# Performance work log

Hardware: AMD Instinct MI355X
Metric: run time of the kernel (lower is better)

Reference implementation:

```python
import jax, jax.numpy as jnp
import numpy as np

N = 100000      # num_nodes (num_users + num_items)
E = 1600000     # directed edges after symmetrization
DIN = 256
HID = 64
DOUT = 64


def setup_inputs() -> dict:
    key = jax.random.key(0)
    k = jax.random.split(key, 4)
    x = jax.random.normal(k[0], (N, DIN), dtype=jnp.float32)
    edge_index = jax.random.randint(k[1], (2, E), 0, N)
    edge_weight = jnp.ones((E,), dtype=jnp.float32)
    W1 = jax.random.normal(k[2], (DIN, HID), dtype=jnp.float32) * (1.0 / np.sqrt(DIN))
    b1 = jnp.zeros((HID,), dtype=jnp.float32)
    W2 = jax.random.normal(k[3], (HID, DOUT), dtype=jnp.float32) * (1.0 / np.sqrt(HID))
    b2 = jnp.zeros((DOUT,), dtype=jnp.float32)
    return {"x": x, "edge_index": edge_index, "edge_weight": edge_weight,
            "W1": W1, "b1": b1, "W2": W2, "b2": b2}


def _gcn_layer(x, W, b, src, dst, ew):
    # PyG GCNConv: h = x @ W; symmetric degree normalization; scatter-add at dst; + bias
    h = x @ W                                             # [N, D_out]
    deg = jax.ops.segment_sum(ew, dst, num_segments=N)    # in-degree w.r.t. edge weights
    dinv = jnp.where(deg > 0, jax.lax.rsqrt(deg), 0.0)    # deg^{-1/2}, inf -> 0
    norm = dinv[src] * ew * dinv[dst]                     # [E_tot]
    msg = h[src] * norm[:, None]                          # gather + scale
    out = jax.ops.segment_sum(msg, dst, num_segments=N)   # scatter-add
    return out + b


def reference(x, edge_index, edge_weight, W1, b1, W2, b2):
    # add self-loops with weight 1 (GCNConv default add_self_loops=True)
    loop = jnp.arange(N, dtype=edge_index.dtype)
    src = jnp.concatenate([edge_index[0], loop])
    dst = jnp.concatenate([edge_index[1], loop])
    ew = jnp.concatenate([edge_weight, jnp.ones((N,), edge_weight.dtype)])
    h = jax.nn.relu(_gcn_layer(x, W1, b1, src, dst, ew))
    return _gcn_layer(h, W2, b2, src, dst, ew)
```

## Files before the change

kernel.cpp:

```cpp
#include <hip/hip_runtime.h>
#include <math.h>


#define GCN_DIN 256
#define GCN_HID 64
#define SCAN_B 1024
#define PCHUNK 4096
#define NBMAX 256

__global__ void count_kernel(const int* __restrict__ dst, int* __restrict__ counts, int E) {
    int e = blockIdx.x * blockDim.x + threadIdx.x;
    if (e < E) atomicAdd(&counts[dst[e]], 1);
}

__global__ __launch_bounds__(SCAN_B) void scan_reduce_kernel(
    const int* __restrict__ counts, int* __restrict__ blockSums, int N)
{
    __shared__ int red[SCAN_B];
    int t = threadIdx.x;
    int i = blockIdx.x * SCAN_B + t;
    red[t] = (i < N) ? counts[i] : 0;
    __syncthreads();
    #pragma unroll
    for (int off = SCAN_B / 2; off > 0; off >>= 1) {
        if (t < off) red[t] += red[t + off];
        __syncthreads();
    }
    if (t == 0) blockSums[blockIdx.x] = red[0];
}

__global__ __launch_bounds__(128) void scan_sums_kernel(
    const int* __restrict__ blockSums, int* __restrict__ blockOff,
    int* __restrict__ rowptr, int B, int N)
{
    __shared__ int s[128];
    int t = threadIdx.x;
    int v = (t < B) ? blockSums[t] : 0;
    s[t] = v;
    __syncthreads();
    #pragma unroll
    for (int off = 1; off < 128; off <<= 1) {
        int a = (t >= off) ? s[t - off] : 0;
        __syncthreads();
        s[t] += a;
        __syncthreads();
    }
    if (t < B) blockOff[t] = s[t] - v;
    if (t == B - 1) rowptr[N] = s[t];
}

__global__ __launch_bounds__(SCAN_B) void scan_final_kernel(
    const int* __restrict__ counts, const int* __restrict__ blockOff,
    int* __restrict__ rowptr, int N)
{
    __shared__ int s[SCAN_B];
    int t = threadIdx.x;
    int i = blockIdx.x * SCAN_B + t;
    int v = (i < N) ? counts[i] : 0;
    s[t] = v;
    __syncthreads();
    for (int off = 1; off < SCAN_B; off <<= 1) {
        int a = (t >= off) ? s[t - off] : 0;
        __syncthreads();
        s[t] += a;
        __syncthreads();
    }
    if (i < N) rowptr[i] = blockOff[blockIdx.x] + s[t] - v;
}

__global__ void bcur_init_kernel(const int* __restrict__ rowptr, int* __restrict__ bucketCursor,
                                 int NB, int N) {
    int b = blockIdx.x * blockDim.x + threadIdx.x;
    if (b < NB) {
        int node = b << 9;
        bucketCursor[b] = rowptr[node < N ? node : N];
    }
}

__global__ __launch_bounds__(256) void partition_kernel(
    const int* __restrict__ src, const int* __restrict__ dst, const float* __restrict__ ew,
    int* __restrict__ bucketCursor, int2* __restrict__ tmp, int E)
{
    __shared__ int hcount[NBMAX];
    __shared__ int hbase[NBMAX];
    __shared__ int hoff[NBMAX];
    const int tid = threadIdx.x;
    const int b0 = blockIdx.x * PCHUNK;
    const int bend = (b0 + PCHUNK < E) ? (b0 + PCHUNK) : E;

    for (int i = tid; i < NBMAX; i += 256) { hcount[i] = 0; hoff[i] = 0; }
    __syncthreads();
    for (int e = b0 + tid; e < bend; e += 256)
        atomicAdd(&hcount[dst[e] >> 9], 1);
    __syncthreads();
    for (int i = tid; i < NBMAX; i += 256)
        if (hcount[i] > 0) hbase[i] = atomicAdd(&bucketCursor[i], hcount[i]);
    __syncthreads();
    for (int e = b0 + tid; e < bend; e += 256) {
        int d = dst[e];
        int b = d >> 9;
        int off = atomicAdd(&hoff[b], 1);
        int key = ((d & 511) << 17) | src[e];
        tmp[hbase[b] + off] = make_int2(key, __float_as_int(ew[e]));
    }
}

__global__ __launch_bounds__(256) void bucket_scatter_kernel(
    const int* __restrict__ rowptr, const int2* __restrict__ tmp,
    int2* __restrict__ comb, int N)
{
    __shared__ int cur[512];
    const int tid = threadIdx.x;
    const int base = blockIdx.x << 9;
    const int nn = (base + 512 < N) ? 512 : (N - base);
    for (int i = tid; i < nn; i += 256) cur[i] = rowptr[base + i];
    __syncthreads();
    const int jb = rowptr[base];
    const int je = rowptr[base + nn];
    for (int j = jb + tid; j < je; j += 256) {
        int2 t = tmp[j];
        int local = t.x >> 17;
        int s = t.x & 0x1FFFF;
        int pos = atomicAdd(&cur[local], 1);
        comb[pos] = make_int2(s, t.y);
    }
}

__global__ void degw_kernel(const int* __restrict__ rowptr, const int2* __restrict__ comb,
                            float* __restrict__ dinv, int N) {
    int n = blockIdx.x * blockDim.x + threadIdx.x;
    if (n >= N) return;
    float s = 1.0f;
    int je = rowptr[n + 1];
    for (int j = rowptr[n]; j < je; ++j) s += __int_as_float(comb[j].y);
    dinv[n] = (s > 0.f) ? (1.0f / sqrtf(s)) : 0.f;
}

__global__ __launch_bounds__(256) void gemm1_kernel(
    const float* __restrict__ x, const float* __restrict__ W,
    const float* __restrict__ dinv, float* __restrict__ g, int N)
{
    __shared__ float xs[32][68];
    __shared__ float ws[32][64];
    const int tid = threadIdx.x;
    const int tx = tid & 15;
    const int ty = tid >> 4;
    const int row0 = blockIdx.x * 64;

    float acc[4][4];
    #pragma unroll
    for (int i = 0; i < 4; ++i)
        #pragma unroll
        for (int j = 0; j < 4; ++j) acc[i][j] = 0.f;

    for (int k0 = 0; k0 < GCN_DIN; k0 += 32) {
        {
            int kc = tid & 7;
            int r  = tid >> 3;
            #pragma unroll
            for (int h = 0; h < 2; ++h) {
                int rr = r + 32 * h;
                int row = row0 + rr;
                float4 v = make_float4(0.f, 0.f, 0.f, 0.f);
                if (row < N) v = *(const float4*)&x[(size_t)row * GCN_DIN + k0 + kc * 4];
                xs[kc * 4 + 0][rr] = v.x;
                xs[kc * 4 + 1][rr] = v.y;
                xs[kc * 4 + 2][rr] = v.z;
                xs[kc * 4 + 3][rr] = v.w;
            }
        }
        {
            int c  = tid & 63;
            int kr = tid >> 6;
            #pragma unroll
            for (int h = 0; h < 8; ++h)
                ws[kr + 4 * h][c] = W[(size_t)(k0 + kr + 4 * h) * 64 + c];
        }
        __syncthreads();
        #pragma unroll
        for (int kk = 0; kk < 32; ++kk) {
            float4 a = *(const float4*)&xs[kk][ty * 4];
            float4 b = *(const float4*)&ws[kk][tx * 4];
            float av[4] = {a.x, a.y, a.z, a.w};
            float bv[4] = {b.x, b.y, b.z, b.w};
            #pragma unroll
            for (int i = 0; i < 4; ++i)
                #pragma unroll
                for (int j = 0; j < 4; ++j)
                    acc[i][j] = fmaf(av[i], bv[j], acc[i][j]);
        }
        __syncthreads();
    }
    #pragma unroll
    for (int i = 0; i < 4; ++i) {
        int row = row0 + ty * 4 + i;
        if (row < N) {
            float dv = dinv[row];
            float4 o = make_float4(dv * acc[i][0], dv * acc[i][1],
                                   dv * acc[i][2], dv * acc[i][3]);
            *(float4*)&g[(size_t)row * 64 + tx * 4] = o;
        }
    }
}

__global__ __launch_bounds__(256) void gemm2_kernel(
    const float* __restrict__ acc1, const float* __restrict__ W,
    const float* __restrict__ dinv, const float* __restrict__ b1,
    float* __restrict__ g, int N)
{
    __shared__ float xs[32][68];
    __shared__ float ws[32][64];
    const int tid = threadIdx.x;
    const int tx = tid & 15;
    const int ty = tid >> 4;
    const int row0 = blockIdx.x * 64;

    float acc[4][4];
    #pragma unroll
    for (int i = 0; i < 4; ++i)
        #pragma unroll
        for (int j = 0; j < 4; ++j) acc[i][j] = 0.f;

    for (int k0 = 0; k0 < GCN_HID; k0 += 32) {
        {
            int kc = tid & 7;
            int r  = tid >> 3;
            float4 bb = *(const float4*)&b1[k0 + kc * 4];
            #pragma unroll
            for (int h = 0; h < 2; ++h) {
                int rr = r + 32 * h;
                int row = row0 + rr;
                float4 v = make_float4(0.f, 0.f, 0.f, 0.f);
                if (row < N) {
                    float dv = dinv[row];
                    float4 hh = *(const float4*)&acc1[(size_t)row * 64 + k0 + kc * 4];
                    v.x = fmaxf(dv * hh.x + bb.x, 0.f);
                    v.y = fmaxf(dv * hh.y + bb.y, 0.f);
                    v.z = fmaxf(dv * hh.z + bb.z, 0.f);
                    v.w = fmaxf(dv * hh.w + bb.w, 0.f);
                }
                xs[kc * 4 + 0][rr] = v.x;
                xs[kc * 4 + 1][rr] = v.y;
                xs[kc * 4 + 2][rr] = v.z;
                xs[kc * 4 + 3][rr] = v.w;
            }
        }
        {
            int c  = tid & 63;
            int kr = tid >> 6;
            #pragma unroll
            for (int h = 0; h < 8; ++h)
                ws[kr + 4 * h][c] = W[(size_t)(k0 + kr + 4 * h) * 64 + c];
        }
        __syncthreads();
        #pragma unroll
        for (int kk = 0; kk < 32; ++kk) {
            float4 a = *(const float4*)&xs[kk][ty * 4];
            float4 b = *(const float4*)&ws[kk][tx * 4];
            float av[4] = {a.x, a.y, a.z, a.w};
            float bv[4] = {b.x, b.y, b.z, b.w};
            #pragma unroll
            for (int i = 0; i < 4; ++i)
                #pragma unroll
                for (int j = 0; j < 4; ++j)
                    acc[i][j] = fmaf(av[i], bv[j], acc[i][j]);
        }
        __syncthreads();
    }
    #pragma unroll
    for (int i = 0; i < 4; ++i) {
        int row = row0 + ty * 4 + i;
        if (row < N) {
            float dv = dinv[row];
            float4 o = make_float4(dv * acc[i][0], dv * acc[i][1],
                                   dv * acc[i][2], dv * acc[i][3]);
            *(float4*)&g[(size_t)row * 64 + tx * 4] = o;
        }
    }
}

__global__ __launch_bounds__(256) void pull_kernel(
    const int* __restrict__ rowptr, const int2* __restrict__ comb,
    const float* __restrict__ g, float* __restrict__ out, int N)
{
    int wid  = (blockIdx.x * blockDim.x + threadIdx.x) >> 6;
    int lane = threadIdx.x & 63;
    if (wid >= N) return;
    int jb = rowptr[wid], je = rowptr[wid + 1];
    float acc = g[(size_t)wid * 64 + lane];
    int j = jb;
    for (; j + 3 < je; j += 4) {
        int2 e0 = comb[j], e1 = comb[j + 1], e2 = comb[j + 2], e3 = comb[j + 3];
        float v0 = g[(size_t)e0.x * 64 + lane];
        float v1 = g[(size_t)e1.x * 64 + lane];
        float v2 = g[(size_t)e2.x * 64 + lane];
        float v3 = g[(size_t)e3.x * 64 + lane];
        acc = fmaf(__int_as_float(e0.y), v0, acc);
        acc = fmaf(__int_as_float(e1.y), v1, acc);
        acc = fmaf(__int_as_float(e2.y), v2, acc);
        acc = fmaf(__int_as_float(e3.y), v3, acc);
    }
    for (; j < je; ++j) {
        int2 e0 = comb[j];
        acc = fmaf(__int_as_float(e0.y), g[(size_t)e0.x * 64 + lane], acc);
    }
    out[(size_t)wid * 64 + lane] = acc;
}

__global__ __launch_bounds__(256) void pull_final_kernel(
    const int* __restrict__ rowptr, const int2* __restrict__ comb,
    const float* __restrict__ g, const float* __restrict__ dinv,
    const float* __restrict__ b2, float* __restrict__ out, int N)
{
    int wid  = (blockIdx.x * blockDim.x + threadIdx.x) >> 6;
    int lane = threadIdx.x & 63;
    if (wid >= N) return;
    int jb = rowptr[wid], je = rowptr[wid + 1];
    float acc = g[(size_t)wid * 64 + lane];
    int j = jb;
    for (; j + 3 < je; j += 4) {
        int2 e0 = comb[j], e1 = comb[j + 1], e2 = comb[j + 2], e3 = comb[j + 3];
        float v0 = g[(size_t)e0.x * 64 + lane];
        float v1 = g[(size_t)e1.x * 64 + lane];
        float v2 = g[(size_t)e2.x * 64 + lane];
        float v3 = g[(size_t)e3.x * 64 + lane];
        acc = fmaf(__int_as_float(e0.y), v0, acc);
        acc = fmaf(__int_as_float(e1.y), v1, acc);
        acc = fmaf(__int_as_float(e2.y), v2, acc);
        acc = fmaf(__int_as_float(e3.y), v3, acc);
    }
    for (; j < je; ++j) {
        int2 e0 = comb[j];
        acc = fmaf(__int_as_float(e0.y), g[(size_t)e0.x * 64 + lane], acc);
    }
    out[(size_t)wid * 64 + lane] = dinv[wid] * acc + b2[lane];
}

extern "C" void kernel_launch(void* const* d_in, const int* in_sizes, int n_in,
                              void* d_out, int out_size, void* d_ws, size_t ws_size,
                              hipStream_t stream) {
    const float* x  = (const float*)d_in[0];
    const int*   ei = (const int*)  d_in[1];
    const float* ew = (const float*)d_in[2];
    const float* W1 = (const float*)d_in[3];
    const float* b1 = (const float*)d_in[4];
    const float* W2 = (const float*)d_in[5];
    const float* b2 = (const float*)d_in[6];
    float* out = (float*)d_out;

    const int N = in_sizes[0] / GCN_DIN;
    const int E = in_sizes[1] / 2;
    const int* src = ei;
    const int* dst = ei + E;
    const int NB = (N + 511) >> 9;

    char* p = (char*)d_ws;
    int2*  comb   = (int2*)p;  p += (size_t)E * sizeof(int2);
    float* B1     = (float*)p; p += (size_t)N * 64 * sizeof(float);
    float* B2     = (float*)p; p += (size_t)N * 64 * sizeof(float);
    float* dinv   = (float*)p; p += (size_t)N * sizeof(float);
    int*   counts = (int*)p;   p += (size_t)N * sizeof(int);
    int*   rowptr = (int*)p;   p += (size_t)(N + 1) * sizeof(int);
    int*   blockSums = (int*)p; p += 128 * sizeof(int);
    int*   blockOff  = (int*)p; p += 128 * sizeof(int);
    int*   bucketCursor = (int*)p; p += NBMAX * sizeof(int);
    int2*  tmp = (int2*)B1;

    const int eBlocks = (E + 255) / 256;
    const int gBlocks = (N + 63) / 64;
    const int wBlocks = (N + 3) / 4;
    const int sBlocks = (N + SCAN_B - 1) / SCAN_B;
    const int pBlocks = (E + PCHUNK - 1) / PCHUNK;

    hipMemsetAsync(counts, 0, (size_t)N * sizeof(int), stream);
    count_kernel<<<eBlocks, 256, 0, stream>>>(dst, counts, E);
    scan_reduce_kernel<<<sBlocks, SCAN_B, 0, stream>>>(counts, blockSums, N);
    scan_sums_kernel<<<1, 128, 0, stream>>>(blockSums, blockOff, rowptr, sBlocks, N);
    scan_final_kernel<<<sBlocks, SCAN_B, 0, stream>>>(counts, blockOff, rowptr, N);
    bcur_init_kernel<<<1, 256, 0, stream>>>(rowptr, bucketCursor, NB, N);
    partition_kernel<<<pBlocks, 256, 0, stream>>>(src, dst, ew, bucketCursor, tmp, E);
    bucket_scatter_kernel<<<NB, 256, 0, stream>>>(rowptr, tmp, comb, N);
    degw_kernel<<<(N + 255) / 256, 256, 0, stream>>>(rowptr, comb, dinv, N);

    gemm1_kernel<<<gBlocks, 256, 0, stream>>>(x, W1, dinv, B1, N);
    pull_kernel<<<wBlocks, 256, 0, stream>>>(rowptr, comb, B1, B2, N);

    gemm2_kernel<<<gBlocks, 256, 0, stream>>>(B2, W2, dinv, b1, B1, N);
    pull_final_kernel<<<wBlocks, 256, 0, stream>>>(rowptr, comb, B1, dinv, b2, out, N);
}
```

Measured before the change: 497.1 us.

## Build CSR via bucket-level counts and fuse rowptr, degree, scatter per bucket

Replaces the per-node count, the three-stage global scan, and the separate degree kernel with a bucket-level histogram and a 256-entry scan. Per-node counts, rowptr, weighted degrees and dinv are then computed inside each bucket's finalize block from the partitioned temp array. This removes several launches, the per-node global atomics and an extra pass over comb. The pull kernels also move to 8-way unrolling with two accumulators to raise memory-level parallelism. The costs are a float atomic on shared memory for the edge-weight sums and a second read of tmp inside the finalize kernel.

```diff
diff --git a/kernel.cpp b/kernel.cpp
--- a/kernel.cpp
+++ b/kernel.cpp
@@ -4,77 +4,40 @@
 
 #define GCN_DIN 256
 #define GCN_HID 64
-#define SCAN_B 1024
 #define PCHUNK 4096
 #define NBMAX 256
 
-__global__ void count_kernel(const int* __restrict__ dst, int* __restrict__ counts, int E) {
-    int e = blockIdx.x * blockDim.x + threadIdx.x;
-    if (e < E) atomicAdd(&counts[dst[e]], 1);
-}
-
-__global__ __launch_bounds__(SCAN_B) void scan_reduce_kernel(
-    const int* __restrict__ counts, int* __restrict__ blockSums, int N)
-{
-    __shared__ int red[SCAN_B];
+__global__ __launch_bounds__(256) void bucket_count_kernel(
+    const int* __restrict__ dst, int* __restrict__ bucketCount, int E)
+{
+    __shared__ int h[NBMAX];
+    for (int i = threadIdx.x; i < NBMAX; i += 256) h[i] = 0;
+    __syncthreads();
+    int stride = gridDim.x * 256;
+    for (int e = blockIdx.x * 256 + threadIdx.x; e < E; e += stride)
+        atomicAdd(&h[dst[e] >> 9], 1);
+    __syncthreads();
+    for (int i = threadIdx.x; i < NBMAX; i += 256)
+        if (h[i]) atomicAdd(&bucketCount[i], h[i]);
+}
+
+__global__ __launch_bounds__(NBMAX) void bucket_scan_kernel(
+    const int* __restrict__ bucketCount, int* __restrict__ bucketBase,
+    int* __restrict__ bucketCursor, int NB)
+{
+    __shared__ int s[NBMAX];
     int t = threadIdx.x;
-    int i = blockIdx.x * SCAN_B + t;
-    red[t] = (i < N) ? counts[i] : 0;
-    __syncthreads();
-    #pragma unroll
-    for (int off = SCAN_B / 2; off > 0; off >>= 1) {
-        if (t < off) red[t] += red[t + off];
-        __syncthreads();
-    }
-    if (t == 0) blockSums[blockIdx.x] = red[0];
-}
-
-__global__ __launch_bounds__(128) void scan_sums_kernel(
-    const int* __restrict__ blockSums, int* __restrict__ blockOff,
-    int* __restrict__ rowptr, int B, int N)
-{
-    __shared__ int s[128];
-    int t = threadIdx.x;
-    int v = (t < B) ? blockSums[t] : 0;
+    int v = (t < NB) ? bucketCount[t] : 0;
     s[t] = v;
     __syncthreads();
-    #pragma unroll
-    for (int off = 1; off < 128; off <<= 1) {
+    for (int off = 1; off < NBMAX; off <<= 1) {
         int a = (t >= off) ? s[t - off] : 0;
         __syncthreads();
         s[t] += a;
         __syncthreads();
     }
-    if (t < B) blockOff[t] = s[t] - v;
-    if (t == B - 1) rowptr[N] = s[t];
-}
-
-__global__ __launch_bounds__(SCAN_B) void scan_final_kernel(
-    const int* __restrict__ counts, const int* __restrict__ blockOff,
-    int* __restrict__ rowptr, int N)
-{
-    __shared__ int s[SCAN_B];
-    int t = threadIdx.x;
-    int i = blockIdx.x * SCAN_B + t;
-    int v = (i < N) ? counts[i] : 0;
-    s[t] = v;
-    __syncthreads();
-    for (int off = 1; off < SCAN_B; off <<= 1) {
-        int a = (t >= off) ? s[t - off] : 0;
-        __syncthreads();
-        s[t] += a;
-        __syncthreads();
-    }
-    if (i < N) rowptr[i] = blockOff[blockIdx.x] + s[t] - v;
-}
-
-__global__ void bcur_init_kernel(const int* __restrict__ rowptr, int* __restrict__ bucketCursor,
-                                 int NB, int N) {
-    int b = blockIdx.x * blockDim.x + threadIdx.x;
-    if (b < NB) {
-        int node = b << 9;
-        bucketCursor[b] = rowptr[node < N ? node : N];
-    }
+    if (t < NB) { int ex = s[t] - v; bucketBase[t] = ex; bucketCursor[t] = ex; }
+    if (t == NB - 1) bucketBase[NB] = s[t];
 }
 
 __global__ __launch_bounds__(256) void partition_kernel(
@@ -105,35 +68,54 @@
     }
 }
 
-__global__ __launch_bounds__(256) void bucket_scatter_kernel(
-    const int* __restrict__ rowptr, const int2* __restrict__ tmp,
-    int2* __restrict__ comb, int N)
-{
-    __shared__ int cur[512];
+__global__ __launch_bounds__(256) void bucket_finalize_kernel(
+    const int* __restrict__ bucketBase, const int2* __restrict__ tmp,
+    int2* __restrict__ comb, int* __restrict__ rowptr, float* __restrict__ dinv,
+    int N, int NB)
+{
+    __shared__ int   cnt[512];
+    __shared__ float ews[512];
+    __shared__ int   sc[512];
+    __shared__ int   cur[512];
     const int tid = threadIdx.x;
-    const int base = blockIdx.x << 9;
+    const int b = blockIdx.x;
+    const int base = b << 9;
     const int nn = (base + 512 < N) ? 512 : (N - base);
-    for (int i = tid; i < nn; i += 256) cur[i] = rowptr[base + i];
-    __syncthreads();
-    const int jb = rowptr[base];
-    const int je = rowptr[base + nn];
+    for (int i = tid; i < 512; i += 256) { cnt[i] = 0; ews[i] = 0.f; }
+    __syncthreads();
+    const int jb = bucketBase[b], je = bucketBase[b + 1];
     for (int j = jb + tid; j < je; j += 256) {
         int2 t = tmp[j];
-        int local = t.x >> 17;
-        int s = t.x & 0x1FFFF;
-        int pos = atomicAdd(&cur[local], 1);
-        comb[pos] = make_int2(s, t.y);
-    }
-}
-
-__global__ void degw_kernel(const int* __restrict__ rowptr, const int2* __restrict__ comb,
-                            float* __restrict__ dinv, int N) {
-    int n = blockIdx.x * blockDim.x + threadIdx.x;
-    if (n >= N) return;
-    float s = 1.0f;
-    int je = rowptr[n + 1];
-    for (int j = rowptr[n]; j < je; ++j) s += __int_as_float(comb[j].y);
-    dinv[n] = (s > 0.f) ? (1.0f / sqrtf(s)) : 0.f;
+        int l = t.x >> 17;
+        atomicAdd(&cnt[l], 1);
+        atomicAdd(&ews[l], __int_as_float(t.y));
+    }
+    __syncthreads();
+    for (int i = tid; i < 512; i += 256) sc[i] = cnt[i];
+    __syncthreads();
+    for (int off = 1; off < 512; off <<= 1) {
+        int i0 = tid, i1 = tid + 256;
+        int v0 = (i0 >= off) ? sc[i0 - off] : 0;
+        int v1 = (i1 >= off) ? sc[i1 - off] : 0;
+        __syncthreads();
+        sc[i0] += v0; sc[i1] += v1;
+        __syncthreads();
+    }
+    for (int i = tid; i < 512; i += 256) cur[i] = sc[i] - cnt[i];
+    __syncthreads();
+    for (int i = tid; i < nn; i += 256) {
+        rowptr[base + i] = jb + cur[i];
+        float s = 1.0f + ews[i];
+        dinv[base + i] = (s > 0.f) ? (1.0f / sqrtf(s)) : 0.f;
+    }
+    if (b == NB - 1 && tid == 0) rowptr[N] = je;
+    __syncthreads();
+    for (int j = jb + tid; j < je; j += 256) {
+        int2 t = tmp[j];
+        int l = t.x >> 17;
+        int pos = jb + atomicAdd(&cur[l], 1);
+        comb[pos] = make_int2(t.x & 0x1FFFF, t.y);
+    }
 }
 
 __global__ __launch_bounds__(256) void gemm1_kernel(
@@ -287,24 +269,34 @@
     int lane = threadIdx.x & 63;
     if (wid >= N) return;
     int jb = rowptr[wid], je = rowptr[wid + 1];
-    float acc = g[(size_t)wid * 64 + lane];
+    float acc0 = g[(size_t)wid * 64 + lane];
+    float acc1 = 0.f;
     int j = jb;
-    for (; j + 3 < je; j += 4) {
-        int2 e0 = comb[j], e1 = comb[j + 1], e2 = comb[j + 2], e3 = comb[j + 3];
+    for (; j + 7 < je; j += 8) {
+        int2 e0 = comb[j],     e1 = comb[j + 1], e2 = comb[j + 2], e3 = comb[j + 3];
+        int2 e4 = comb[j + 4], e5 = comb[j + 5], e6 = comb[j + 6], e7 = comb[j + 7];
         float v0 = g[(size_t)e0.x * 64 + lane];
         float v1 = g[(size_t)e1.x * 64 + lane];
         float v2 = g[(size_t)e2.x * 64 + lane];
         float v3 = g[(size_t)e3.x * 64 + lane];
-        acc = fmaf(__int_as_float(e0.y), v0, acc);
-        acc = fmaf(__int_as_float(e1.y), v1, acc);
-        acc = fmaf(__int_as_float(e2.y), v2, acc);
-        acc = fmaf(__int_as_float(e3.y), v3, acc);
+        float v4 = g[(size_t)e4.x * 64 + lane];
+        float v5 = g[(size_t)e5.x * 64 + lane];
+        float v6 = g[(size_t)e6.x * 64 + lane];
+        float v7 = g[(size_t)e7.x * 64 + lane];
+        acc0 = fmaf(__int_as_float(e0.y), v0, acc0);
+        acc1 = fmaf(__int_as_float(e1.y), v1, acc1);
+        acc0 = fmaf(__int_as_float(e2.y), v2, acc0);
+        acc1 = fmaf(__int_as_float(e3.y), v3, acc1);
+        acc0 = fmaf(__int_as_float(e4.y), v4, acc0);
+        acc1 = fmaf(__int_as_float(e5.y), v5, acc1);
+        acc0 = fmaf(__int_as_float(e6.y), v6, acc0);
+        acc1 = fmaf(__int_as_float(e7.y), v7, acc1);
     }
     for (; j < je; ++j) {
         int2 e0 = comb[j];
-        acc = fmaf(__int_as_float(e0.y), g[(size_t)e0.x * 64 + lane], acc);
-    }
-    out[(size_t)wid * 64 + lane] = acc;
+        acc0 = fmaf(__int_as_float(e0.y), g[(size_t)e0.x * 64 + lane], acc0);
+    }
+    out[(size_t)wid * 64 + lane] = acc0 + acc1;
 }
 
 __global__ __launch_bounds__(256) void pull_final_kernel(
@@ -316,24 +308,34 @@
     int lane = threadIdx.x & 63;
     if (wid >= N) return;
     int jb = rowptr[wid], je = rowptr[wid + 1];
-    float acc = g[(size_t)wid * 64 + lane];
+    float acc0 = g[(size_t)wid * 64 + lane];
+    float acc1 = 0.f;
     int j = jb;
-    for (; j + 3 < je; j += 4) {
-        int2 e0 = comb[j], e1 = comb[j + 1], e2 = comb[j + 2], e3 = comb[j + 3];
+    for (; j + 7 < je; j += 8) {
+        int2 e0 = comb[j],     e1 = comb[j + 1], e2 = comb[j + 2], e3 = comb[j + 3];
+        int2 e4 = comb[j + 4], e5 = comb[j + 5], e6 = comb[j + 6], e7 = comb[j + 7];
         float v0 = g[(size_t)e0.x * 64 + lane];
         float v1 = g[(size_t)e1.x * 64 + lane];
         float v2 = g[(size_t)e2.x * 64 + lane];
         float v3 = g[(size_t)e3.x * 64 + lane];
-        acc = fmaf(__int_as_float(e0.y), v0, acc);
-        acc = fmaf(__int_as_float(e1.y), v1, acc);
-        acc = fmaf(__int_as_float(e2.y), v2, acc);
-        acc = fmaf(__int_as_float(e3.y), v3, acc);
+        float v4 = g[(size_t)e4.x * 64 + lane];
+        float v5 = g[(size_t)e5.x * 64 + lane];
+        float v6 = g[(size_t)e6.x * 64 + lane];
+        float v7 = g[(size_t)e7.x * 64 + lane];
+        acc0 = fmaf(__int_as_float(e0.y), v0, acc0);
+        acc1 = fmaf(__int_as_float(e1.y), v1, acc1);
+        acc0 = fmaf(__int_as_float(e2.y), v2, acc0);
+        acc1 = fmaf(__int_as_float(e3.y), v3, acc1);
+        acc0 = fmaf(__int_as_float(e4.y), v4, acc0);
+        acc1 = fmaf(__int_as_float(e5.y), v5, acc1);
+        acc0 = fmaf(__int_as_float(e6.y), v6, acc0);
+        acc1 = fmaf(__int_as_float(e7.y), v7, acc1);
     }
     for (; j < je; ++j) {
         int2 e0 = comb[j];
-        acc = fmaf(__int_as_float(e0.y), g[(size_t)e0.x * 64 + lane], acc);
-    }
-    out[(size_t)wid * 64 + lane] = dinv[wid] * acc + b2[lane];
+        acc0 = fmaf(__int_as_float(e0.y), g[(size_t)e0.x * 64 + lane], acc0);
+    }
+    out[(size_t)wid * 64 + lane] = dinv[wid] * (acc0 + acc1) + b2[lane];
 }
 
 extern "C" void kernel_launch(void* const* d_in, const int* in_sizes, int n_in,
@@ -359,28 +361,21 @@
     float* B1     = (float*)p; p += (size_t)N * 64 * sizeof(float);
     float* B2     = (float*)p; p += (size_t)N * 64 * sizeof(float);
     float* dinv   = (float*)p; p += (size_t)N * sizeof(float);
-    int*   counts = (int*)p;   p += (size_t)N * sizeof(int);
     int*   rowptr = (int*)p;   p += (size_t)(N + 1) * sizeof(int);
-    int*   blockSums = (int*)p; p += 128 * sizeof(int);
-    int*   blockOff  = (int*)p; p += 128 * sizeof(int);
+    int*   bucketCount  = (int*)p; p += NBMAX * sizeof(int);
+    int*   bucketBase   = (int*)p; p += (NBMAX + 1) * sizeof(int);
     int*   bucketCursor = (int*)p; p += NBMAX * sizeof(int);
     int2*  tmp = (int2*)B1;
 
-    const int eBlocks = (E + 255) / 256;
     const int gBlocks = (N + 63) / 64;
     const int wBlocks = (N + 3) / 4;
-    const int sBlocks = (N + SCAN_B - 1) / SCAN_B;
     const int pBlocks = (E + PCHUNK - 1) / PCHUNK;
 
-    hipMemsetAsync(counts, 0, (size_t)N * sizeof(int), stream);
-    count_kernel<<<eBlocks, 256, 0, stream>>>(dst, counts, E);
-    scan_reduce_kernel<<<sBlocks, SCAN_B, 0, stream>>>(counts, blockSums, N);
-    scan_sums_kernel<<<1, 128, 0, stream>>>(blockSums, blockOff, rowptr, sBlocks, N);
-    scan_final_kernel<<<sBlocks, SCAN_B, 0, stream>>>(counts, blockOff, rowptr, N);
-    bcur_init_kernel<<<1, 256, 0, stream>>>(rowptr, bucketCursor, NB, N);
+    hipMemsetAsync(bucketCount, 0, NBMAX * sizeof(int), stream);
+    bucket_count_kernel<<<512, 256, 0, stream>>>(dst, bucketCount, E);
+    bucket_scan_kernel<<<1, NBMAX, 0, stream>>>(bucketCount, bucketBase, bucketCursor, NB);
     partition_kernel<<<pBlocks, 256, 0, stream>>>(src, dst, ew, bucketCursor, tmp, E);
-    bucket_scatter_kernel<<<NB, 256, 0, stream>>>(rowptr, tmp, comb, N);
-    degw_kernel<<<(N + 255) / 256, 256, 0, stream>>>(rowptr, comb, dinv, N);
+    bucket_finalize_kernel<<<NB, 256, 0, stream>>>(bucketBase, tmp, comb, rowptr, dinv, N, NB);
 
     gemm1_kernel<<<gBlocks, 256, 0, stream>>>(x, W1, dinv, B1, N);
     pull_kernel<<<wBlocks, 256, 0, stream>>>(rowptr, comb, B1, B2, N);
```

Result: faster. 461.9 us (-7.1%).
